# Optimization experiments

Measured on AMD Instinct MI355X. Metric: run time of the kernel, lower is better.

The kernel has to match this reference:

```python
import jax, jax.numpy as jnp
import numpy as np

EPS = 1e-5  # BatchNorm2d default eps


def _resize_bilinear(x, out_h, out_w):
    # PyTorch F.interpolate(mode='bilinear', align_corners=False, antialias=False):
    # input coord = (out + 0.5)/scale - 0.5  ->  translation = 0.5*(scale-1)
    b, c, h, w = x.shape
    sh, sw = out_h / h, out_w / w
    scale = jnp.array([sh, sw], dtype=jnp.float32)
    trans = jnp.array([0.5 * (sh - 1.0), 0.5 * (sw - 1.0)], dtype=jnp.float32)
    return jax.image.scale_and_translate(
        x, (b, c, out_h, out_w), (2, 3), scale, trans,
        method='linear', antialias=False)


def setup_inputs() -> dict:
    key = jax.random.key(0)
    ks = jax.random.split(key, 6)
    B, C, IC, H, W = 4, 64, 16, 128, 128
    init = lambda k, shape, fan_in: (
        jax.random.normal(k, shape, jnp.float32) / np.float32(np.sqrt(fan_in)))
    return {
        'x': jax.random.normal(ks[0], (B, C, H, W), jnp.float32),
        'g_w': init(ks[1], (IC, C), C), 'g_b': jnp.zeros((IC,), jnp.float32),
        'theta_w': init(ks[2], (IC, C), C), 'theta_b': jnp.zeros((IC,), jnp.float32),
        'phi_w': init(ks[3], (IC, C), C), 'phi_b': jnp.zeros((IC,), jnp.float32),
        'out_w': init(ks[4], (C, IC), IC), 'out_b': jnp.zeros((C,), jnp.float32),
        'bn_gamma': jnp.ones((C,), jnp.float32), 'bn_beta': jnp.zeros((C,), jnp.float32),
    }


def reference(x, g_w, g_b, theta_w, theta_b, phi_w, phi_b,
              out_w, out_b, bn_gamma, bn_beta):
    b, c, h, w = x.shape
    dh, dw = h // 2, w // 2          # downsample_factor = 0.5
    xd = _resize_bilinear(x, dh, dw).reshape(b, c, dh * dw)  # [b,C,N]

    # 1x1 convs == per-pixel linear projections
    g_x = jnp.einsum('bcn,oc->bno', xd, g_w) + g_b          # [b,N,IC]
    th = jnp.einsum('bcn,oc->bno', xd, theta_w) + theta_b   # [b,N,IC]
    ph = jnp.einsum('bcn,oc->bon', xd, phi_w) + phi_b[None, :, None]  # [b,IC,N]

    f = jnp.einsum('bni,bim->bnm', th, ph)   # [b,N,N] score matrix (no scaling)
    attn = jax.nn.softmax(f, axis=-1)
    y = jnp.einsum('bnm,bmi->bni', attn, g_x)               # [b,N,IC]
    y = y.transpose(0, 2, 1).reshape(b, -1, dh, dw)         # [b,IC,dh,dw]

    y = _resize_bilinear(y, h, w)                            # upsample back
    y = jnp.einsum('bihw,ci->bchw', y, out_w) + out_b[None, :, None, None]

    z = x + y
    # BatchNorm2d in (default) training mode: biased batch stats over (B,H,W)
    mean = jnp.mean(z, axis=(0, 2, 3))
    var = jnp.var(z, axis=(0, 2, 3))
    zn = (z - mean[None, :, None, None]) * jax.lax.rsqrt(var + EPS)[None, :, None, None]
    return zn * bn_gamma[None, :, None, None] + bn_beta[None, :, None, None]
```

## Files before the change

kernel.cpp:

```cpp
#include <hip/hip_runtime.h>
#include <math.h>

#define NB 4
#define NC 64
#define NI 16
#define NH 128
#define NW 128
#define ND 64
#define NN 4096
#define KSPL 4

#define LOG2E 1.4426950408889634f

using bfrag  = __attribute__((ext_vector_type(8))) short;
using bfrag4 = __attribute__((ext_vector_type(4))) short;
using ffrag  = __attribute__((ext_vector_type(4))) float;

#if __has_builtin(__builtin_amdgcn_exp2f)
#define EXP2(x) __builtin_amdgcn_exp2f(x)
#else
#define EXP2(x) exp2f(x)
#endif

__device__ __forceinline__ unsigned bf16rne(float f) {
    unsigned u = __float_as_uint(f);
    return (u + 0x7FFFu + ((u >> 16) & 1u)) >> 16;
}
__device__ __forceinline__ unsigned pk_rne(float lo, float hi) {
    return bf16rne(lo) | (bf16rne(hi) << 16);
}
__device__ __forceinline__ unsigned pk_trunc(float lo, float hi) {
    return (__float_as_uint(lo) >> 16) | (__float_as_uint(hi) & 0xFFFF0000u);
}

__device__ __forceinline__ ffrag mfma_qk(bfrag4 a, bfrag4 b, ffrag c) {
#if __has_builtin(__builtin_amdgcn_mfma_f32_16x16x16bf16_1k)
    return __builtin_amdgcn_mfma_f32_16x16x16bf16_1k(a, b, c, 0, 0, 0);
#else
    union { bfrag4 h[2]; bfrag v; } ua, ub;
    bfrag4 zz = {0, 0, 0, 0};
    ua.h[0] = a; ua.h[1] = zz;
    ub.h[0] = b; ub.h[1] = zz;
    return __builtin_amdgcn_mfma_f32_16x16x32_bf16(ua.v, ub.v, c, 0, 0, 0);
#endif
}

extern "C" __global__ __launch_bounds__(256)
void k_proj(const float* __restrict__ x,
            const float* __restrict__ gw, const float* __restrict__ gb,
            const float* __restrict__ tw, const float* __restrict__ tb,
            const float* __restrict__ pw, const float* __restrict__ pb,
            uint2* __restrict__ th_sw, uint2* __restrict__ phi_sw,
            uint4* __restrict__ g_sw, float* __restrict__ shstats)
{
    __shared__ float swt[NC][48];
    __shared__ float sb[48];
    __shared__ float red[3][64][49];
    __shared__ __align__(16) unsigned short gtile[16][64];
    int tid = threadIdx.x;
    int b = blockIdx.x >> 6, i = blockIdx.x & 63;
    if (blockIdx.x == 0) {
#pragma unroll
        for (int k = 0; k < 4; ++k) shstats[tid + k*256] = 0.f;
    }
    for (int idx = tid; idx < NI*NC; idx += 256) {
        int o = idx >> 6, c = idx & 63;
        swt[c][o]      = tw[idx];
        swt[c][16 + o] = pw[idx];
        swt[c][32 + o] = gw[idx];
    }
    if (tid < 16) { sb[tid] = tb[tid]; sb[16+tid] = pb[tid]; sb[32+tid] = gb[tid]; }
    __syncthreads();

    int j = tid & 63, part = tid >> 6;
    const float* xp = x + (((size_t)(b*NC + part*16))*NH + (2*i+1))*NW + (2*j+1);
    float a[48];
#pragma unroll
    for (int k = 0; k < 48; ++k) a[k] = 0.f;
    for (int cc = 0; cc < 16; ++cc) {
        float xd = xp[(size_t)cc*NH*NW];
        const float* wr = swt[part*16 + cc];
#pragma unroll
        for (int k = 0; k < 48; ++k) a[k] += xd*wr[k];
    }
    if (part != 0) {
#pragma unroll
        for (int k = 0; k < 48; ++k) red[part-1][j][k] = a[k];
    }
    __syncthreads();
    if (part == 0) {
        float aT[16], aP[16], aG[16];
#pragma unroll
        for (int o = 0; o < 16; ++o) {
            float vT = a[o]    + red[0][j][o]    + red[1][j][o]    + red[2][j][o];
            float vP = a[16+o] + red[0][j][16+o] + red[1][j][16+o] + red[2][j][16+o];
            float vG = a[32+o] + red[0][j][32+o] + red[1][j][32+o] + red[2][j][32+o];
            aT[o] = (vT + sb[o]) * LOG2E;
            aP[o] =  vP + sb[16+o];
            aG[o] =  vG + sb[32+o];
        }
        int q = i*64 + j;
        int n = j & 15;
        size_t qtile = (size_t)b*256 + (q >> 4);
#pragma unroll
        for (int qd = 0; qd < 4; ++qd)
            th_sw[qtile*64 + qd*16 + n] =
                make_uint2(pk_rne(aT[4*qd], aT[4*qd+1]), pk_rne(aT[4*qd+2], aT[4*qd+3]));
        int wk = j & 31;
        int f = (wk >> 2) & 1;
        int r = ((wk >> 3) << 2) | (wk & 3);
        size_t kgrp = (size_t)b*256 + (q >> 5)*2 + f;
#pragma unroll
        for (int qd = 0; qd < 4; ++qd)
            phi_sw[kgrp*64 + qd*16 + r] =
                make_uint2(pk_rne(aP[4*qd], aP[4*qd+1]), pk_rne(aP[4*qd+2], aP[4*qd+3]));
#pragma unroll
        for (int o = 0; o < 16; ++o) gtile[o][j] = (unsigned short)bf16rne(aG[o]);
    }
    __syncthreads();
    if (tid < 128) {
        int c2 = tid >> 6, L = tid & 63;
        int n = L & 15, q8 = L >> 4;
        const uint4* src = (const uint4*)&gtile[n][c2*32 + q8*8];
        g_sw[((size_t)b*128 + i*2 + c2)*64 + L] = *src;
    }
}

extern "C" __global__ __launch_bounds__(256, 4)
void k_attn(const uint2* __restrict__ th_sw, const uint2* __restrict__ phi_sw,
            const uint4* __restrict__ g_sw, float* __restrict__ accp,
            float* __restrict__ lp)
{
    __shared__ __align__(16) uint2 sphi[16*64];
    __shared__ __align__(16) uint4 sg[8*64];
    int tid = threadIdx.x;
    int wave = tid >> 6, lane = tid & 63;
    int quad = lane >> 4, low = lane & 15;
    int qgroup = blockIdx.x, ks = blockIdx.y, b = blockIdx.z;

    union { uint2 u; bfrag4 f; } thu;
    thu.u = th_sw[((size_t)b*256 + qgroup*4 + wave)*64 + lane];
    bfrag4 theta = thu.f;

    ffrag yacc = {0.f, 0.f, 0.f, 0.f};
    const ffrag zf = {0.f, 0.f, 0.f, 0.f};
    float lacc = 0.f;

    for (int chunk = 0; chunk < 4; ++chunk) {
        __syncthreads();
        const uint4* srcP = (const uint4*)(phi_sw + ((size_t)b*256 + ks*64 + chunk*16)*64);
        const uint4* srcG = g_sw + ((size_t)b*128 + ks*32 + chunk*8)*64;
        ((uint4*)sphi)[tid]       = srcP[tid];
        ((uint4*)sphi)[256 + tid] = srcP[256 + tid];
        sg[tid]       = srcG[tid];
        sg[256 + tid] = srcG[256 + tid];
        __syncthreads();

        const bfrag4* sphiF = (const bfrag4*)sphi;
        const bfrag*  sgF   = (const bfrag*)sg;
#pragma unroll
        for (int s = 0; s < 8; ++s) {
            bfrag4 pA = sphiF[(2*s+0)*64 + lane];
            bfrag4 pB = sphiF[(2*s+1)*64 + lane];
            bfrag  vf = sgF[s*64 + lane];
            ffrag sA = mfma_qk(pA, theta, zf);
            ffrag sB = mfma_qk(pB, theta, zf);
            float eA0 = EXP2(sA[0]), eA1 = EXP2(sA[1]), eA2 = EXP2(sA[2]), eA3 = EXP2(sA[3]);
            float eB0 = EXP2(sB[0]), eB1 = EXP2(sB[1]), eB2 = EXP2(sB[2]), eB3 = EXP2(sB[3]);
            lacc += ((eA0+eA1) + (eA2+eA3)) + ((eB0+eB1) + (eB2+eB3));
            union { unsigned u[4]; bfrag f; } pu;
            pu.u[0] = pk_trunc(eA0, eA1);
            pu.u[1] = pk_trunc(eA2, eA3);
            pu.u[2] = pk_trunc(eB0, eB1);
            pu.u[3] = pk_trunc(eB2, eB3);
            yacc = __builtin_amdgcn_mfma_f32_16x16x32_bf16(pu.f, vf, yacc, 0, 0, 0);
        }
    }

    lacc += __shfl_xor(lacc, 16, 64);
    lacc += __shfl_xor(lacc, 32, 64);

    int qbase = qgroup*64 + wave*16;
    size_t pbase = ((size_t)ks*NB + b)*NN;
#pragma unroll
    for (int reg = 0; reg < 4; ++reg)
        accp[(pbase + qbase + quad*4 + reg)*16 + low] = yacc[reg];
    if (lane < 16) lp[pbase + qbase + lane] = lacc;
}

extern "C" __global__ __launch_bounds__(256)
void k_outz(const float* __restrict__ accp, const float* __restrict__ lp,
            const float* __restrict__ x, const float* __restrict__ ow,
            const float* __restrict__ ob, float* __restrict__ z,
            float* __restrict__ shstats)
{
    __shared__ float slab[32*257];
    __shared__ float syd[2][NI][ND];
    __shared__ float sl[2][ND];
    __shared__ float swv[NC*NI];
    __shared__ float sbv[NC];
    int t = threadIdx.x;
    int hp = blockIdx.x, b = blockIdx.y;
    for (int idx = t; idx < NC*NI; idx += 256) swv[idx] = ow[idx];
    if (t < NC) sbv[t] = ob[t];

    {
        int r = t >> 7, col = (t >> 1) & 63, half = t & 1;
        int row = (r == 0) ? (hp > 0 ? hp-1 : 0) : hp;
        int q = row*64 + col;
        float4 a0 = make_float4(0.f,0.f,0.f,0.f), a1 = a0;
        float lsum = 0.f;
        for (int ks = 0; ks < KSPL; ++ks) {
            const float4* ap = (const float4*)accp + (((size_t)ks*NB + b)*NN + q)*4 + 2*half;
            float4 v0 = ap[0], v1 = ap[1];
            a0.x += v0.x; a0.y += v0.y; a0.z += v0.z; a0.w += v0.w;
            a1.x += v1.x; a1.y += v1.y; a1.z += v1.z; a1.w += v1.w;
            if (half == 0) lsum += lp[((size_t)ks*NB + b)*NN + q];
        }
        if (half == 0) sl[r][col] = lsum;
        __syncthreads();
        float inv = 1.f / sl[r][col];
        int i0 = 8*half;
        syd[r][i0+0][col] = a0.x*inv; syd[r][i0+1][col] = a0.y*inv;
        syd[r][i0+2][col] = a0.z*inv; syd[r][i0+3][col] = a0.w*inv;
        syd[r][i0+4][col] = a1.x*inv; syd[r][i0+5][col] = a1.y*inv;
        syd[r][i0+6][col] = a1.z*inv; syd[r][i0+7][col] = a1.w*inv;
    }
    __syncthreads();

    int w = t & 127, hsel = t >> 7;
    int h = 2*hp + hsel;
    float wh0 = hsel ? 0.f : 0.5f;
    float wh1 = hsel ? 1.f : 0.5f;
    int c0, c1; float wc0, wc1;
    if (w & 1) { c0 = c1 = (w-1) >> 1; wc0 = 1.f; wc1 = 0.f; }
    else       { c1 = w >> 1; c0 = c1 ? c1-1 : 0; wc0 = 0.5f; wc1 = 0.5f; }
    float yv[16];
#pragma unroll
    for (int i = 0; i < 16; ++i)
        yv[i] = wh0*(wc0*syd[0][i][c0] + wc1*syd[0][i][c1])
              + wh1*(wc0*syd[1][i][c0] + wc1*syd[1][i][c1]);

    const float* xb = x + (((size_t)(b*NC))*NH + h)*NW + w;
    float* zb       = z + (((size_t)(b*NC))*NH + h)*NW + w;
    float zreg[64];
#pragma unroll
    for (int c = 0; c < NC; ++c) {
        const float* wr = swv + c*16;
        float acc = sbv[c];
#pragma unroll
        for (int i = 0; i < 16; ++i) acc += wr[i]*yv[i];
        zreg[c] = xb[(size_t)c*NH*NW] + acc;
        zb[(size_t)c*NH*NW] = zreg[c];
    }

    float* shadow = shstats + ((((unsigned)b << 6) + (unsigned)hp) & 7u)*128;
    int c32 = t >> 3, oct = t & 7;
#pragma unroll
    for (int half = 0; half < 2; ++half) {
        __syncthreads();
#pragma unroll
        for (int cc = 0; cc < 32; ++cc)
            slab[cc*257 + t] = zreg[half*32 + cc];
        __syncthreads();
        float s = 0.f, s2 = 0.f;
#pragma unroll
        for (int k = 0; k < 32; ++k) {
            int p2 = oct*32 + ((k + 4*oct) & 31);
            float v = slab[c32*257 + p2];
            s += v; s2 += v*v;
        }
        s  += __shfl_xor(s, 1);  s  += __shfl_xor(s, 2);  s  += __shfl_xor(s, 4);
        s2 += __shfl_xor(s2, 1); s2 += __shfl_xor(s2, 2); s2 += __shfl_xor(s2, 4);
        if (oct == 0) atomicAdd(shadow + half*32 + c32, s);
        if (oct == 1) atomicAdd(shadow + 64 + half*32 + c32, s2);
    }
}

extern "C" __global__ __launch_bounds__(256)
void k_norm(const float* __restrict__ z, const float* __restrict__ shstats,
            const float* __restrict__ gamma, const float* __restrict__ beta,
            float* __restrict__ out)
{
    __shared__ float sga[NC], sbe[NC];
    int t = threadIdx.x;
    if (t < NC) {
        float s = 0.f, s2 = 0.f;
#pragma unroll
        for (int sh = 0; sh < 8; ++sh) {
            s  += shstats[sh*128 + t];
            s2 += shstats[sh*128 + 64 + t];
        }
        const float inv_cnt = 1.f/65536.f;
        float mean = s*inv_cnt;
        float var  = s2*inv_cnt - mean*mean;
        float rs = rsqrtf(var + 1e-5f);
        float ga = gamma[t]*rs;
        sga[t] = ga;
        sbe[t] = beta[t] - mean*ga;
    }
    __syncthreads();
#pragma unroll
    for (int it = 0; it < 4; ++it) {
        size_t i4 = ((size_t)blockIdx.x*4 + it)*256 + t;
        int c = (int)((i4 >> 12) & 63);
        float4 v = ((const float4*)z)[i4];
        float ga = sga[c], be = sbe[c];
        ((float4*)out)[i4] = make_float4(v.x*ga+be, v.y*ga+be, v.z*ga+be, v.w*ga+be);
    }
}

extern "C" void kernel_launch(void* const* d_in, const int* in_sizes, int n_in,
                              void* d_out, int out_size, void* d_ws, size_t ws_size,
                              hipStream_t stream)
{
    const float* x     = (const float*)d_in[0];
    const float* gw    = (const float*)d_in[1];
    const float* gb    = (const float*)d_in[2];
    const float* tw    = (const float*)d_in[3];
    const float* tb    = (const float*)d_in[4];
    const float* pw    = (const float*)d_in[5];
    const float* pb    = (const float*)d_in[6];
    const float* ow    = (const float*)d_in[7];
    const float* ob    = (const float*)d_in[8];
    const float* gamma = (const float*)d_in[9];
    const float* beta  = (const float*)d_in[10];
    float* out = (float*)d_out;

    char* wsb = (char*)d_ws;
    uint2* th_sw  = (uint2*)(wsb);
    uint2* phi_sw = (uint2*)(wsb + (512u<<10));
    uint4* g_sw   = (uint4*)(wsb + (1024u<<10));
    float* lp     = (float*)(wsb + (1536u<<10));
    float* shst   = (float*)(wsb + (1792u<<10));
    float* accp   = (float*)(wsb + (2048u<<10));
    float* z      = (float*)(wsb + (6u<<20) + (256u<<10));

    k_proj<<<256, 256, 0, stream>>>(x, gw, gb, tw, tb, pw, pb,
                                    th_sw, phi_sw, g_sw, shst);
    k_attn<<<dim3(64, KSPL, NB), 256, 0, stream>>>(th_sw, phi_sw, g_sw, accp, lp);
    k_outz<<<dim3(64, NB), 256, 0, stream>>>(accp, lp, x, ow, ob, z, shst);
    k_norm<<<1024, 256, 0, stream>>>(z, shst, gamma, beta, out);
}
```

Baseline: 127.0 us.

## Fuse BatchNorm apply into output kernel via grid-wide atomic barrier

Removes the separate normalization kernel and the intermediate z buffer. After each block of k_outz adds its channel sums, it joins a software grid barrier built on an atomic counter (reset in k_proj), then reads the batch statistics and writes normalized output straight from registers. This saves a full write and reread of z (16 MB) and one launch. It relies on all 256 blocks being resident at once, which the 256-CU device should allow, but a spin-wait adds deadlock risk.

```diff
diff --git a/kernel.cpp b/kernel.cpp
--- a/kernel.cpp
+++ b/kernel.cpp
@@ -51,7 +51,8 @@
             const float* __restrict__ tw, const float* __restrict__ tb,
             const float* __restrict__ pw, const float* __restrict__ pb,
             uint2* __restrict__ th_sw, uint2* __restrict__ phi_sw,
-            uint4* __restrict__ g_sw, float* __restrict__ shstats)
+            uint4* __restrict__ g_sw, float* __restrict__ shstats,
+            unsigned* __restrict__ bar)
 {
     __shared__ float swt[NC][48];
     __shared__ float sb[48];
@@ -62,6 +63,8 @@
     if (blockIdx.x == 0) {
 #pragma unroll
         for (int k = 0; k < 4; ++k) shstats[tid + k*256] = 0.f;
+        if (tid == 0)
+            __hip_atomic_store(bar, 0u, __ATOMIC_RELAXED, __HIP_MEMORY_SCOPE_AGENT);
     }
     for (int idx = tid; idx < NI*NC; idx += 256) {
         int o = idx >> 6, c = idx & 63;
@@ -191,14 +194,16 @@
 extern "C" __global__ __launch_bounds__(256)
 void k_outz(const float* __restrict__ accp, const float* __restrict__ lp,
             const float* __restrict__ x, const float* __restrict__ ow,
-            const float* __restrict__ ob, float* __restrict__ z,
-            float* __restrict__ shstats)
+            const float* __restrict__ ob, const float* __restrict__ gamma,
+            const float* __restrict__ beta, float* __restrict__ shstats,
+            unsigned* __restrict__ bar, float* __restrict__ out)
 {
     __shared__ float slab[32*257];
     __shared__ float syd[2][NI][ND];
     __shared__ float sl[2][ND];
     __shared__ float swv[NC*NI];
     __shared__ float sbv[NC];
+    __shared__ float sga[NC], sbe[NC];
     int t = threadIdx.x;
     int hp = blockIdx.x, b = blockIdx.y;
     for (int idx = t; idx < NC*NI; idx += 256) swv[idx] = ow[idx];
@@ -242,7 +247,6 @@
               + wh1*(wc0*syd[1][i][c0] + wc1*syd[1][i][c1]);
 
     const float* xb = x + (((size_t)(b*NC))*NH + h)*NW + w;
-    float* zb       = z + (((size_t)(b*NC))*NH + h)*NW + w;
     float zreg[64];
 #pragma unroll
     for (int c = 0; c < NC; ++c) {
@@ -251,7 +255,6 @@
 #pragma unroll
         for (int i = 0; i < 16; ++i) acc += wr[i]*yv[i];
         zreg[c] = xb[(size_t)c*NH*NW] + acc;
-        zb[(size_t)c*NH*NW] = zreg[c];
     }
 
     float* shadow = shstats + ((((unsigned)b << 6) + (unsigned)hp) & 7u)*128;
@@ -275,21 +278,23 @@
         if (oct == 0) atomicAdd(shadow + half*32 + c32, s);
         if (oct == 1) atomicAdd(shadow + 64 + half*32 + c32, s2);
     }
-}
-
-extern "C" __global__ __launch_bounds__(256)
-void k_norm(const float* __restrict__ z, const float* __restrict__ shstats,
-            const float* __restrict__ gamma, const float* __restrict__ beta,
-            float* __restrict__ out)
-{
-    __shared__ float sga[NC], sbe[NC];
-    int t = threadIdx.x;
+
+    __syncthreads();
+    if (t == 0) {
+        __threadfence();
+        __hip_atomic_fetch_add(bar, 1u, __ATOMIC_ACQ_REL, __HIP_MEMORY_SCOPE_AGENT);
+        while (__hip_atomic_load(bar, __ATOMIC_ACQUIRE, __HIP_MEMORY_SCOPE_AGENT) < 256u) {
+            __builtin_amdgcn_s_sleep(8);
+        }
+    }
+    __syncthreads();
+
     if (t < NC) {
         float s = 0.f, s2 = 0.f;
 #pragma unroll
         for (int sh = 0; sh < 8; ++sh) {
-            s  += shstats[sh*128 + t];
-            s2 += shstats[sh*128 + 64 + t];
+            s  += __hip_atomic_load(shstats + sh*128 + t,      __ATOMIC_RELAXED, __HIP_MEMORY_SCOPE_AGENT);
+            s2 += __hip_atomic_load(shstats + sh*128 + 64 + t, __ATOMIC_RELAXED, __HIP_MEMORY_SCOPE_AGENT);
         }
         const float inv_cnt = 1.f/65536.f;
         float mean = s*inv_cnt;
@@ -300,14 +305,10 @@
         sbe[t] = beta[t] - mean*ga;
     }
     __syncthreads();
-#pragma unroll
-    for (int it = 0; it < 4; ++it) {
-        size_t i4 = ((size_t)blockIdx.x*4 + it)*256 + t;
-        int c = (int)((i4 >> 12) & 63);
-        float4 v = ((const float4*)z)[i4];
-        float ga = sga[c], be = sbe[c];
-        ((float4*)out)[i4] = make_float4(v.x*ga+be, v.y*ga+be, v.z*ga+be, v.w*ga+be);
-    }
+    float* ob2 = out + (((size_t)(b*NC))*NH + h)*NW + w;
+#pragma unroll
+    for (int c = 0; c < NC; ++c)
+        ob2[(size_t)c*NH*NW] = zreg[c]*sga[c] + sbe[c];
 }
 
 extern "C" void kernel_launch(void* const* d_in, const int* in_sizes, int n_in,
@@ -328,17 +329,17 @@
     float* out = (float*)d_out;
 
     char* wsb = (char*)d_ws;
-    uint2* th_sw  = (uint2*)(wsb);
-    uint2* phi_sw = (uint2*)(wsb + (512u<<10));
-    uint4* g_sw   = (uint4*)(wsb + (1024u<<10));
-    float* lp     = (float*)(wsb + (1536u<<10));
-    float* shst   = (float*)(wsb + (1792u<<10));
-    float* accp   = (float*)(wsb + (2048u<<10));
-    float* z      = (float*)(wsb + (6u<<20) + (256u<<10));
+    uint2*    th_sw  = (uint2*)(wsb);
+    uint2*    phi_sw = (uint2*)(wsb + (512u<<10));
+    uint4*    g_sw   = (uint4*)(wsb + (1024u<<10));
+    float*    lp     = (float*)(wsb + (1536u<<10));
+    float*    shst   = (float*)(wsb + (1792u<<10));
+    unsigned* bar    = (unsigned*)(wsb + (1796u<<10));
+    float*    accp   = (float*)(wsb + (2048u<<10));
 
     k_proj<<<256, 256, 0, stream>>>(x, gw, gb, tw, tb, pw, pb,
-                                    th_sw, phi_sw, g_sw, shst);
+                                    th_sw, phi_sw, g_sw, shst, bar);
     k_attn<<<dim3(64, KSPL, NB), 256, 0, stream>>>(th_sw, phi_sw, g_sw, accp, lp);
-    k_outz<<<dim3(64, NB), 256, 0, stream>>>(accp, lp, x, ow, ob, z, shst);
-    k_norm<<<1024, 256, 0, stream>>>(z, shst, gamma, beta, out);
-}
+    k_outz<<<dim3(64, NB), 256, 0, stream>>>(accp, lp, x, ow, ob, gamma, beta,
+                                             shst, bar, out);
+}
```

Result: slower. 187.3 us (+47.6%).
